# Optimization experiments

Hardware: AMD Instinct MI355X
Metric: run time of the kernel (lower is better)

Reference implementation:

```python
import jax, jax.numpy as jnp
import numpy as np

FILTER_LENGTHS = (2, 4)  # from module: self.filter_length = [2, 4]


def _get_conv(signal, b, h, l, d_k, conv, w):
    # signal: [b, h*d_k, l] (raw reshape of [b,h,l,d_k], matching torch .reshape)
    f = max(FILTER_LENGTHS)
    pad = f // 2
    padded = jnp.pad(signal, ((0, 0), (0, 0), (pad, pad)))  # [b, d, l+f]
    # unfold(-1, f, 1)[:, :, :l, :] -> sliding windows, keep first l
    idx = jnp.arange(l)[:, None] + jnp.arange(f)[None, :]  # [l, f]
    seq = padded[:, :, idx]  # [b, d, l, f]
    # dynamic filter-length selection: w_f = filter_lengths * w, pick argmax
    f_s = jnp.asarray(FILTER_LENGTHS, dtype=signal.dtype)
    ind = jnp.argmax(f_s * w)
    chosen_len = jnp.asarray(FILTER_LENGTHS)[ind]
    mask = (jnp.arange(f) < chosen_len).astype(signal.dtype)  # [f]
    seq = seq * mask  # broadcast over [b, d, l, f]
    # depthwise-ish conv via einsum, then raw reshape (b, l, h*d_k) -> (b, h, l, d_k)
    out = jnp.einsum('bdlf,dof->blo', seq, conv)
    return out.reshape(b, h, l, d_k)


def reference(Q, K, V, attn_mask, conv_q, conv_k, w):
    b, h, l, d_k = Q.shape
    Qc = _get_conv(Q.reshape(b, h * d_k, l), b, h, l, d_k, conv_q, w) + Q
    Kc = _get_conv(K.reshape(b, h * d_k, l), b, h, l, d_k, conv_k, w) + K
    scores = jnp.einsum('bhqd,bhkd->bhqk', Qc, Kc) / np.sqrt(d_k).astype(Q.dtype)
    attn = jax.nn.softmax(scores, axis=-1)
    context = jnp.einsum('bhqk,bhkd->bhqd', attn, V)
    return context, attn


def setup_inputs() -> dict:
    key = jax.random.key(0)
    ks = jax.random.split(key, 6)
    b, h, l, d_k = 4, 8, 2048, 64
    d = h * d_k
    f = max(FILTER_LENGTHS)
    return {
        'Q': jax.random.normal(ks[0], (b, h, l, d_k), dtype=jnp.float32),
        'K': jax.random.normal(ks[1], (b, h, l, d_k), dtype=jnp.float32),
        'V': jax.random.normal(ks[2], (b, h, l, d_k), dtype=jnp.float32),
        'attn_mask': jnp.zeros((b, 1, l, l), dtype=bool),  # unused by forward
        'conv_q': jax.random.normal(ks[3], (d, d, f), dtype=jnp.float32),
        'conv_k': jax.random.normal(ks[4], (d, d, f), dtype=jnp.float32),
        'w': jax.random.normal(ks[5], (2,), dtype=jnp.float32),
    }
```

## Files before the change

### kernel.cpp

```cpp
#include <hip/hip_runtime.h>

typedef _Float16 f16;
typedef _Float16 f16x8 __attribute__((ext_vector_type(8)));
typedef float f32x16 __attribute__((ext_vector_type(16)));

#define MFMA32(A, B, C) __builtin_amdgcn_mfma_f32_32x32x16_f16(A, B, C, 0, 0, 0)

constexpr int Bb = 4, Hh = 8, Ll = 2048, Dk = 64, Dm = 512, BH = 32;
constexpr int LP = 2052;

constexpr size_t NW  = (size_t)512 * 2048;
constexpr size_t NST = (size_t)Bb * LP * 512;
constexpr size_t NFF = (size_t)BH * 64 * 4 * 64 * 8;
constexpr size_t NVF = (size_t)BH * 2 * 128 * 64 * 8;

constexpr size_t OFF_W  = 256;
constexpr size_t OFF_ST = OFF_W + 4 * NW * sizeof(f16);
constexpr size_t OFF_FF = OFF_ST + 4 * NST * sizeof(f16);
constexpr size_t OFF_VF = OFF_FF + 4 * NFF * sizeof(f16);

#define QSCALE 0.1803368801111204f

__device__ __forceinline__ void gload_lds16(const void* g, void* l) {
    __builtin_amdgcn_global_load_lds((const __attribute__((address_space(1))) unsigned int*)g,
                                     (__attribute__((address_space(3))) unsigned int*)l, 16, 0, 0);
}

__global__ void kprep_w(const float* __restrict__ convq, const float* __restrict__ convk,
                        const float* __restrict__ w, int* __restrict__ flag,
                        f16* __restrict__ wqh, f16* __restrict__ wql,
                        f16* __restrict__ wkh, f16* __restrict__ wkl) {
    const int len = (4.f * w[1] > 2.f * w[0]) ? 4 : 2;
    if (blockIdx.x == 0 && blockIdx.y == 0 && threadIdx.x == 0) *flag = len;
    int tid = blockIdx.x * 256 + threadIdx.x;
    int o = tid >> 9, c = tid & 511;
    const float* conv = blockIdx.y ? convk : convq;
    f16* dh = blockIdx.y ? wkh : wqh;
    f16* dl = blockIdx.y ? wkl : wql;
    const float4 v = *(const float4*)(conv + ((size_t)c * 512 + o) * 4);
    float vv[4] = {v.x, v.y, v.z, v.w};
#pragma unroll
    for (int f = 0; f < 4; ++f) {
        float x = (f < len) ? vv[f] : 0.f;
        f16 hi = (f16)x;
        f16 lo = (f16)(x - (float)hi);
        size_t idx = (size_t)o * 2048 + (f << 9) + c;
        dh[idx] = hi; dl[idx] = lo;
    }
}

__global__ void kprep_s(const float* __restrict__ Q, const float* __restrict__ K,
                        f16* __restrict__ stqh, f16* __restrict__ stql,
                        f16* __restrict__ stkh, f16* __restrict__ stkl) {
    __shared__ float tile[64][65];
    int z = blockIdx.z;
    int tensor = z >> 2, b = z & 3;
    const float* src = (tensor ? K : Q) + (size_t)b * Dm * Ll;
    f16* dh = (tensor ? stkh : stqh) + (size_t)b * LP * Dm;
    f16* dl = (tensor ? stkl : stql) + (size_t)b * LP * Dm;
    int j0 = blockIdx.x * 64, c0 = blockIdx.y * 64;
    int tl = threadIdx.x & 63, tg = threadIdx.x >> 6;
#pragma unroll
    for (int r = 0; r < 16; ++r) {
        int cl = (r << 2) + tg;
        int tabs = j0 + tl - 2;
        float v = (tabs >= 0 && tabs < Ll) ? src[(size_t)(c0 + cl) * Ll + tabs] : 0.f;
        tile[cl][tl] = v;
    }
    __syncthreads();
#pragma unroll
    for (int r = 0; r < 16; ++r) {
        int jl = (r << 2) + tg;
        int j = j0 + jl;
        if (j < LP) {
            float v = tile[tl][jl];
            f16 hi = (f16)v;
            f16 lo = (f16)(v - (float)hi);
            dh[(size_t)j * Dm + c0 + tl] = hi;
            dl[(size_t)j * Dm + c0 + tl] = lo;
        }
    }
}

__global__ void kprep_v(const float* __restrict__ V, f16* __restrict__ vf) {
    int bh = blockIdx.y, l0 = blockIdx.x * 128;
    int tid = threadIdx.x;
    const float* src = V + (size_t)bh * Ll * Dk;
#pragma unroll
    for (int s = 0; s < 4; ++s) {
        int g = s * 4 + (tid >> 6);
        int lane = tid & 63;
        int l16s = g >> 1, db = g & 1;
        int khalf = lane >> 5, lane31 = lane & 31;
        int d = db * 32 + lane31;
        f16x8 out;
#pragma unroll
        for (int j = 0; j < 8; ++j) {
            int l = l0 + l16s * 16 + khalf * 8 + j;
            out[j] = (f16)src[(size_t)l * Dk + d];
        }
        size_t idx = ((((size_t)bh * 2 + db) * 128 + (l0 >> 4) + l16s) * 64 + lane) * 8;
        *(f16x8*)(vf + idx) = out;
    }
}

__global__ __launch_bounds__(256, 2) void kconv(
    const float* __restrict__ Q, const float* __restrict__ K, const int* __restrict__ flag,
    const f16* __restrict__ stqh, const f16* __restrict__ stql,
    const f16* __restrict__ stkh, const f16* __restrict__ stkl,
    const f16* __restrict__ wqh, const f16* __restrict__ wql,
    const f16* __restrict__ wkh, const f16* __restrict__ wkl,
    f16* __restrict__ ffhq, f16* __restrict__ fflq,
    f16* __restrict__ ffhk, f16* __restrict__ fflk) {
    __shared__ f16 At[128 * 64], Bt[128 * 64];
    int id = blockIdx.x;
    int oTile = id & 3, tensor = (id >> 2) & 1;
    int tt = (id >> 3) & 15, b = (id >> 7) & 3;
    int tid = threadIdx.x;
    int wave = tid >> 6, lane = tid & 63;
    int wm = wave >> 1, wn = wave & 1;
    int lane31 = lane & 31, khalf = lane >> 5;
    int t0 = tt * 128, o0 = oTile * 128;
    const f16* sh = (tensor ? stkh : stqh) + (size_t)b * LP * Dm;
    const f16* sl = (tensor ? stkl : stql) + (size_t)b * LP * Dm;
    const f16* wh = tensor ? wkh : wqh;
    const f16* wl = tensor ? wkl : wql;
    const float* src = (tensor ? K : Q) + (size_t)b * Hh * Ll * Dk;
    f16* dh = (tensor ? ffhk : ffhq);
    f16* dl = (tensor ? fflk : fflq);
    const float scale = tensor ? 1.f : QSCALE;
    const int klen = (*flag) << 9;
    const int iters = (3 * klen) >> 6;

    f32x16 acc[2][2];
#pragma unroll
    for (int i = 0; i < 2; ++i)
#pragma unroll
        for (int j = 0; j < 2; ++j)
#pragma unroll
            for (int r = 0; r < 16; ++r) acc[i][j][r] = 0.f;

    for (int it = 0; it < iters; ++it) {
        int kp = it << 6;
        int p = (kp >= 2 * klen) ? 2 : (kp >= klen ? 1 : 0);
        int k0 = kp - p * klen;
        int f = k0 >> 9, c0 = k0 & 511;
        const f16* srcA = (p == 2) ? sl : sh;
        const f16* srcB = (p == 1) ? wl : wh;
        __syncthreads();
#pragma unroll
        for (int c = 0; c < 4; ++c) {
            int s = c * 256 + tid;
            int row = s >> 3;
            int gk = ((s & 7) ^ (row & 7)) * 8;
            gload_lds16(srcA + (size_t)(t0 + f + row) * 512 + c0 + gk, &At[s * 8]);
            gload_lds16(srcB + (size_t)(o0 + row) * 2048 + k0 + gk, &Bt[s * 8]);
        }
        __syncthreads();
#pragma unroll
        for (int kk = 0; kk < 4; ++kk) {
            int cc = (kk << 1) + khalf;
            f16x8 av[2], bv[2];
#pragma unroll
            for (int i = 0; i < 2; ++i) {
                int row = wm * 64 + i * 32 + lane31;
                av[i] = *(const f16x8*)&At[(row * 8 + (cc ^ (row & 7))) * 8];
            }
#pragma unroll
            for (int j = 0; j < 2; ++j) {
                int row = wn * 64 + j * 32 + lane31;
                bv[j] = *(const f16x8*)&Bt[(row * 8 + (cc ^ (row & 7))) * 8];
            }
#pragma unroll
            for (int i = 0; i < 2; ++i)
#pragma unroll
                for (int j = 0; j < 2; ++j)
                    acc[i][j] = MFMA32(av[i], bv[j], acc[i][j]);
        }
    }
#pragma unroll
    for (int i = 0; i < 2; ++i)
#pragma unroll
        for (int j = 0; j < 2; ++j)
#pragma unroll
            for (int r = 0; r < 16; ++r) {
                int trow = t0 + wm * 64 + i * 32 + (r & 3) + ((r >> 2) << 3) + (khalf << 2);
                int ocol = o0 + wn * 64 + j * 32 + lane31;
                int h = trow >> 8;
                int l = ((trow & 255) << 3) + (ocol >> 6);
                int d = ocol & 63;
                float v2 = (acc[i][j][r] + src[((size_t)h * Ll + l) * Dk + d]) * scale;
                f16 hi = (f16)v2;
                f16 lo = (f16)(v2 - (float)hi);
                size_t idx = ((((size_t)(b * 8 + h) * 64 + (l >> 5)) * 4 + (d >> 4)) * 64
                              + ((d >> 3) & 1) * 32 + (l & 31)) * 8 + (d & 7);
                dh[idx] = hi; dl[idx] = lo;
            }
}

__global__ __launch_bounds__(256, 4) void kattn(
    const f16* __restrict__ qfh, const f16* __restrict__ qfl,
    const f16* __restrict__ kfh, const f16* __restrict__ kfl,
    const f16* __restrict__ vf,
    float* __restrict__ ctx_out, float* __restrict__ attn_out) {
    __shared__ __align__(16) char smem[16384];
    float (*combuf)[32][64] = (float (*)[32][64])smem;
    f16 (*ptile)[32][40] = (f16 (*)[32][40])smem;
    int id = blockIdx.x;
    int bh = (id & 7) * 4 + (id >> 8);
    int qt = (id >> 3) & 31;
    int wave = threadIdx.x >> 6, lane = threadIdx.x & 63;
    int qg = wave >> 1, kg = wave & 1;
    int lane31 = lane & 31, khalf = lane >> 5;
    int q0 = qt * 64 + qg * 32;

    f16x8 a_h[4], a_l[4];
    {
        size_t qb = ((size_t)bh * 64 + qt * 2 + qg) * 4;
#pragma unroll
        for (int ks = 0; ks < 4; ++ks) {
            a_h[ks] = *(const f16x8*)(qfh + ((qb + ks) * 64 + lane) * 8);
            a_l[ks] = *(const f16x8*)(qfl + ((qb + ks) * 64 + lane) * 8);
        }
    }
    const f16* kbh = kfh + (size_t)bh * 131072;
    const f16* kbl = kfl + (size_t)bh * 131072;
    const int ch0 = kg * 32, ch1 = ch0 + 32;

    float m[16], s[16];
#pragma unroll
    for (int r = 0; r < 16; ++r) { m[r] = -3.0e38f; s[r] = 0.f; }

#pragma unroll 2
    for (int ch = ch0; ch < ch1; ++ch) {
        f32x16 acc;
#pragma unroll
        for (int r = 0; r < 16; ++r) acc[r] = 0.f;
        size_t kb = (size_t)ch * 2048 + lane * 8;
#pragma unroll
        for (int ks = 0; ks < 4; ++ks) {
            f16x8 kh8 = *(const f16x8*)(kbh + kb + ks * 512);
            f16x8 kl8 = *(const f16x8*)(kbl + kb + ks * 512);
            acc = MFMA32(a_h[ks], kh8, acc);
            acc = MFMA32(a_h[ks], kl8, acc);
            acc = MFMA32(a_l[ks], kh8, acc);
        }
#pragma unroll
        for (int r = 0; r < 16; ++r) {
            float v = acc[r];
            float d = v - m[r];
            float e = exp2f(-fabsf(d));
            bool gt = d > 0.f;
            s[r] = gt ? __fmaf_rn(s[r], e, 1.f) : (s[r] + e);
            m[r] = gt ? v : m[r];
        }
    }
#pragma unroll
    for (int r = 0; r < 16; ++r) {
        float mm = m[r], ss = s[r];
#pragma unroll
        for (int off = 1; off < 32; off <<= 1) {
            float mo = __shfl_xor(mm, off, 64);
            float so = __shfl_xor(ss, off, 64);
            float mn = fmaxf(mm, mo);
            ss = ss * exp2f(mm - mn) + so * exp2f(mo - mn);
            mm = mn;
        }
        m[r] = mm; s[r] = ss;
    }
    if (kg == 1) {
#pragma unroll
        for (int r = 0; r < 16; ++r) {
            combuf[qg][r][lane] = m[r];
            combuf[qg][16 + r][lane] = s[r];
        }
    }
    __syncthreads();
    if (kg == 0) {
#pragma unroll
        for (int r = 0; r < 16; ++r) {
            float m1 = combuf[qg][r][lane];
            float s1 = combuf[qg][16 + r][lane];
            float mn = fmaxf(m[r], m1);
            float ss = s[r] * exp2f(m[r] - mn) + s1 * exp2f(m1 - mn);
            m[r] = mn; s[r] = 1.f / ss;
            combuf[qg][r][lane] = mn;
            combuf[qg][16 + r][lane] = s[r];
        }
    }
    __syncthreads();
    if (kg == 1) {
#pragma unroll
        for (int r = 0; r < 16; ++r) {
            m[r] = combuf[qg][r][lane];
            s[r] = combuf[qg][16 + r][lane];
        }
    }
    __syncthreads();

    f32x16 ctx[2];
#pragma unroll
    for (int n = 0; n < 2; ++n)
#pragma unroll
        for (int r = 0; r < 16; ++r) ctx[n][r] = 0.f;

    const size_t base_q = ((size_t)bh * Ll + q0) * Ll + lane31;

    for (int ch = ch0; ch < ch1; ++ch) {
        f32x16 acc;
#pragma unroll
        for (int r = 0; r < 16; ++r) acc[r] = 0.f;
        size_t kb = (size_t)ch * 2048 + lane * 8;
#pragma unroll
        for (int ks = 0; ks < 4; ++ks) {
            f16x8 kh8 = *(const f16x8*)(kbh + kb + ks * 512);
            f16x8 kl8 = *(const f16x8*)(kbl + kb + ks * 512);
            acc = MFMA32(a_h[ks], kh8, acc);
            acc = MFMA32(a_h[ks], kl8, acc);
            acc = MFMA32(a_l[ks], kh8, acc);
        }
#pragma unroll
        for (int r = 0; r < 16; ++r) {
            float p = exp2f(acc[r] - m[r]) * s[r];
            int row = (r & 3) + ((r >> 2) << 3) + (khalf << 2);
            attn_out[base_q + (size_t)row * Ll + ch * 32] = p;
            ptile[wave][row][lane31] = (f16)p;
        }
        __asm__ volatile("s_waitcnt lgkmcnt(0)" ::: "memory");
#pragma unroll
        for (int ks2 = 0; ks2 < 2; ++ks2) {
            f16x8 pa = *(const f16x8*)&ptile[wave][lane31][ks2 * 16 + khalf * 8];
#pragma unroll
            for (int n = 0; n < 2; ++n) {
                size_t off = ((((size_t)bh * 2 + n) * 128 + ch * 2 + ks2) * 64 + lane) * 8;
                f16x8 vb = *(const f16x8*)(vf + off);
                ctx[n] = MFMA32(pa, vb, ctx[n]);
            }
        }
    }
    __syncthreads();
    if (kg == 1) {
#pragma unroll
        for (int n = 0; n < 2; ++n)
#pragma unroll
            for (int r = 0; r < 16; ++r) combuf[qg][n * 16 + r][lane] = ctx[n][r];
    }
    __syncthreads();
    if (kg == 0) {
#pragma unroll
        for (int n = 0; n < 2; ++n)
#pragma unroll
            for (int r = 0; r < 16; ++r) {
                float v = ctx[n][r] + combuf[qg][n * 16 + r][lane];
                int row = (r & 3) + ((r >> 2) << 3) + (khalf << 2);
                ctx_out[((size_t)bh * Ll + q0 + row) * Dk + n * 32 + lane31] = v;
            }
    }
}

extern "C" void kernel_launch(void* const* d_in, const int* in_sizes, int n_in,
                              void* d_out, int out_size, void* d_ws, size_t ws_size,
                              hipStream_t stream) {
    const float* Q = (const float*)d_in[0];
    const float* K = (const float*)d_in[1];
    const float* V = (const float*)d_in[2];
    const float* convq = (const float*)d_in[4];
    const float* convk = (const float*)d_in[5];
    const float* w = (const float*)d_in[6];

    char* ws = (char*)d_ws;
    int* flag = (int*)ws;
    f16* wqh = (f16*)(ws + OFF_W);
    f16* wql = wqh + NW;
    f16* wkh = wql + NW;
    f16* wkl = wkh + NW;
    f16* stqh = (f16*)(ws + OFF_ST);
    f16* stql = stqh + NST;
    f16* stkh = stql + NST;
    f16* stkl = stkh + NST;
    f16* ffhq = (f16*)(ws + OFF_FF);
    f16* fflq = ffhq + NFF;
    f16* ffhk = fflq + NFF;
    f16* fflk = ffhk + NFF;
    f16* vf = (f16*)(ws + OFF_VF);

    float* ctx_out = (float*)d_out;
    float* attn_out = ctx_out + (size_t)BH * Ll * Dk;

    kprep_w<<<dim3(1024, 2), 256, 0, stream>>>(convq, convk, w, flag, wqh, wql, wkh, wkl);
    kprep_s<<<dim3(33, 8, 8), 256, 0, stream>>>(Q, K, stqh, stql, stkh, stkl);
    kprep_v<<<dim3(16, 32), 256, 0, stream>>>(V, vf);
    kconv<<<dim3(512), 256, 0, stream>>>(Q, K, flag, stqh, stql, stkh, stkl,
                                         wqh, wql, wkh, wkl, ffhq, fflq, ffhk, fflk);
    kattn<<<dim3(1024), 256, 0, stream>>>(ffhq, fflq, ffhk, fflk, vf, ctx_out, attn_out);
}
```

Baseline: 1.081 ms.

## Merge prep kernels, double-buffer conv GEMM, pair chunks and vectorize attn stores

Merges the three preprocessing kernels into one launch that dispatches on block index. The conv GEMM gets double-buffered LDS with the next stage's loads issued before compute, and its block-to-tile mapping is remapped. The attention kernel now processes two 32-key chunks per iteration with a combined online-softmax update. Probabilities are staged in an fp32 LDS tile so the attn output is written with float4 row-contiguous stores instead of scattered scalar stores. The occupancy hint drops from 4 to 3 blocks per CU, and the larger LDS use may reduce occupancy.

```diff
diff --git a/kernel.cpp b/kernel.cpp
--- a/kernel.cpp
+++ b/kernel.cpp
@@ -26,81 +26,88 @@
                                      (__attribute__((address_space(3))) unsigned int*)l, 16, 0, 0);
 }
 
-__global__ void kprep_w(const float* __restrict__ convq, const float* __restrict__ convk,
-                        const float* __restrict__ w, int* __restrict__ flag,
-                        f16* __restrict__ wqh, f16* __restrict__ wql,
-                        f16* __restrict__ wkh, f16* __restrict__ wkl) {
-    const int len = (4.f * w[1] > 2.f * w[0]) ? 4 : 2;
-    if (blockIdx.x == 0 && blockIdx.y == 0 && threadIdx.x == 0) *flag = len;
-    int tid = blockIdx.x * 256 + threadIdx.x;
-    int o = tid >> 9, c = tid & 511;
-    const float* conv = blockIdx.y ? convk : convq;
-    f16* dh = blockIdx.y ? wkh : wqh;
-    f16* dl = blockIdx.y ? wkl : wql;
-    const float4 v = *(const float4*)(conv + ((size_t)c * 512 + o) * 4);
-    float vv[4] = {v.x, v.y, v.z, v.w};
-#pragma unroll
-    for (int f = 0; f < 4; ++f) {
-        float x = (f < len) ? vv[f] : 0.f;
-        f16 hi = (f16)x;
-        f16 lo = (f16)(x - (float)hi);
-        size_t idx = (size_t)o * 2048 + (f << 9) + c;
-        dh[idx] = hi; dl[idx] = lo;
-    }
-}
-
-__global__ void kprep_s(const float* __restrict__ Q, const float* __restrict__ K,
-                        f16* __restrict__ stqh, f16* __restrict__ stql,
-                        f16* __restrict__ stkh, f16* __restrict__ stkl) {
+__global__ void kprep(const float* __restrict__ Q, const float* __restrict__ K,
+                      const float* __restrict__ V,
+                      const float* __restrict__ convq, const float* __restrict__ convk,
+                      const float* __restrict__ w, int* __restrict__ flag,
+                      f16* __restrict__ wqh, f16* __restrict__ wql,
+                      f16* __restrict__ wkh, f16* __restrict__ wkl,
+                      f16* __restrict__ stqh, f16* __restrict__ stql,
+                      f16* __restrict__ stkh, f16* __restrict__ stkl,
+                      f16* __restrict__ vf) {
     __shared__ float tile[64][65];
-    int z = blockIdx.z;
-    int tensor = z >> 2, b = z & 3;
-    const float* src = (tensor ? K : Q) + (size_t)b * Dm * Ll;
-    f16* dh = (tensor ? stkh : stqh) + (size_t)b * LP * Dm;
-    f16* dl = (tensor ? stkl : stql) + (size_t)b * LP * Dm;
-    int j0 = blockIdx.x * 64, c0 = blockIdx.y * 64;
-    int tl = threadIdx.x & 63, tg = threadIdx.x >> 6;
-#pragma unroll
-    for (int r = 0; r < 16; ++r) {
-        int cl = (r << 2) + tg;
-        int tabs = j0 + tl - 2;
-        float v = (tabs >= 0 && tabs < Ll) ? src[(size_t)(c0 + cl) * Ll + tabs] : 0.f;
-        tile[cl][tl] = v;
-    }
-    __syncthreads();
-#pragma unroll
-    for (int r = 0; r < 16; ++r) {
-        int jl = (r << 2) + tg;
-        int j = j0 + jl;
-        if (j < LP) {
-            float v = tile[tl][jl];
-            f16 hi = (f16)v;
-            f16 lo = (f16)(v - (float)hi);
-            dh[(size_t)j * Dm + c0 + tl] = hi;
-            dl[(size_t)j * Dm + c0 + tl] = lo;
-        }
-    }
-}
-
-__global__ void kprep_v(const float* __restrict__ V, f16* __restrict__ vf) {
-    int bh = blockIdx.y, l0 = blockIdx.x * 128;
-    int tid = threadIdx.x;
-    const float* src = V + (size_t)bh * Ll * Dk;
-#pragma unroll
-    for (int s = 0; s < 4; ++s) {
-        int g = s * 4 + (tid >> 6);
-        int lane = tid & 63;
-        int l16s = g >> 1, db = g & 1;
-        int khalf = lane >> 5, lane31 = lane & 31;
-        int d = db * 32 + lane31;
-        f16x8 out;
-#pragma unroll
-        for (int j = 0; j < 8; ++j) {
-            int l = l0 + l16s * 16 + khalf * 8 + j;
-            out[j] = (f16)src[(size_t)l * Dk + d];
-        }
-        size_t idx = ((((size_t)bh * 2 + db) * 128 + (l0 >> 4) + l16s) * 64 + lane) * 8;
-        *(f16x8*)(vf + idx) = out;
+    int id = blockIdx.x;
+    if (id < 2048) {
+        const int len = (4.f * w[1] > 2.f * w[0]) ? 4 : 2;
+        if (id == 0 && threadIdx.x == 0) *flag = len;
+        int part = id >> 10;
+        int tid = (id & 1023) * 256 + threadIdx.x;
+        int o = tid >> 9, c = tid & 511;
+        const float* conv = part ? convk : convq;
+        f16* dh = part ? wkh : wqh;
+        f16* dl = part ? wkl : wql;
+        const float4 v = *(const float4*)(conv + ((size_t)c * 512 + o) * 4);
+        float vv[4] = {v.x, v.y, v.z, v.w};
+#pragma unroll
+        for (int f = 0; f < 4; ++f) {
+            float x = (f < len) ? vv[f] : 0.f;
+            f16 hi = (f16)x;
+            f16 lo = (f16)(x - (float)hi);
+            size_t idx = (size_t)o * 2048 + (f << 9) + c;
+            dh[idx] = hi; dl[idx] = lo;
+        }
+    } else if (id < 4160) {
+        int sid = id - 2048;
+        int jb = sid % 33;
+        int rest = sid / 33;
+        int cb = rest & 7, z = rest >> 3;
+        int tensor = z >> 2, b = z & 3;
+        const float* src = (tensor ? K : Q) + (size_t)b * Dm * Ll;
+        f16* dh = (tensor ? stkh : stqh) + (size_t)b * LP * Dm;
+        f16* dl = (tensor ? stkl : stql) + (size_t)b * LP * Dm;
+        int j0 = jb * 64, c0 = cb * 64;
+        int tl = threadIdx.x & 63, tg = threadIdx.x >> 6;
+#pragma unroll
+        for (int r = 0; r < 16; ++r) {
+            int cl = (r << 2) + tg;
+            int tabs = j0 + tl - 2;
+            float v = (tabs >= 0 && tabs < Ll) ? src[(size_t)(c0 + cl) * Ll + tabs] : 0.f;
+            tile[cl][tl] = v;
+        }
+        __syncthreads();
+#pragma unroll
+        for (int r = 0; r < 16; ++r) {
+            int jl = (r << 2) + tg;
+            int j = j0 + jl;
+            if (j < LP) {
+                float v = tile[tl][jl];
+                f16 hi = (f16)v;
+                f16 lo = (f16)(v - (float)hi);
+                dh[(size_t)j * Dm + c0 + tl] = hi;
+                dl[(size_t)j * Dm + c0 + tl] = lo;
+            }
+        }
+    } else {
+        int vid = id - 4160;
+        int bh = vid >> 4, l0 = (vid & 15) * 128;
+        int tid = threadIdx.x;
+        const float* src = V + (size_t)bh * Ll * Dk;
+#pragma unroll
+        for (int s = 0; s < 4; ++s) {
+            int g = s * 4 + (tid >> 6);
+            int lane = tid & 63;
+            int l16s = g >> 1, db = g & 1;
+            int khalf = lane >> 5, lane31 = lane & 31;
+            int d = db * 32 + lane31;
+            f16x8 out;
+#pragma unroll
+            for (int j = 0; j < 8; ++j) {
+                int l = l0 + l16s * 16 + khalf * 8 + j;
+                out[j] = (f16)src[(size_t)l * Dk + d];
+            }
+            size_t idx = ((((size_t)bh * 2 + db) * 128 + (l0 >> 4) + l16s) * 64 + lane) * 8;
+            *(f16x8*)(vf + idx) = out;
+        }
     }
 }
 
@@ -112,10 +119,11 @@
     const f16* __restrict__ wkh, const f16* __restrict__ wkl,
     f16* __restrict__ ffhq, f16* __restrict__ fflq,
     f16* __restrict__ ffhk, f16* __restrict__ fflk) {
-    __shared__ f16 At[128 * 64], Bt[128 * 64];
+    __shared__ f16 At[2][128 * 64], Bt[2][128 * 64];
     int id = blockIdx.x;
-    int oTile = id & 3, tensor = (id >> 2) & 1;
-    int tt = (id >> 3) & 15, b = (id >> 7) & 3;
+    int oTile = (id >> 3) & 3;
+    int gg = (id >> 5) * 8 + (id & 7);
+    int tt = gg & 15, b = (gg >> 4) & 3, tensor = gg >> 6;
     int tid = threadIdx.x;
     int wave = tid >> 6, lane = tid & 63;
     int wm = wave >> 1, wn = wave & 1;
@@ -140,23 +148,27 @@
 #pragma unroll
             for (int r = 0; r < 16; ++r) acc[i][j][r] = 0.f;
 
-    for (int it = 0; it < iters; ++it) {
+    auto stage = [&](int it, int buf) {
         int kp = it << 6;
         int p = (kp >= 2 * klen) ? 2 : (kp >= klen ? 1 : 0);
         int k0 = kp - p * klen;
         int f = k0 >> 9, c0 = k0 & 511;
-        const f16* srcA = (p == 2) ? sl : sh;
-        const f16* srcB = (p == 1) ? wl : wh;
+        const f16* sA = (p == 2) ? sl : sh;
+        const f16* sB = (p == 1) ? wl : wh;
+#pragma unroll
+        for (int c = 0; c < 4; ++c) {
+            int sIdx = c * 256 + tid;
+            int row = sIdx >> 3;
+            int gk = ((sIdx & 7) ^ (row & 7)) * 8;
+            gload_lds16(sA + (size_t)(t0 + f + row) * 512 + c0 + gk, &At[buf][sIdx * 8]);
+            gload_lds16(sB + (size_t)(o0 + row) * 2048 + k0 + gk, &Bt[buf][sIdx * 8]);
+        }
+    };
+    stage(0, 0);
+    for (int it = 0; it < iters; ++it) {
+        int cur = it & 1;
         __syncthreads();
-#pragma unroll
-        for (int c = 0; c < 4; ++c) {
-            int s = c * 256 + tid;
-            int row = s >> 3;
-            int gk = ((s & 7) ^ (row & 7)) * 8;
-            gload_lds16(srcA + (size_t)(t0 + f + row) * 512 + c0 + gk, &At[s * 8]);
-            gload_lds16(srcB + (size_t)(o0 + row) * 2048 + k0 + gk, &Bt[s * 8]);
-        }
-        __syncthreads();
+        if (it + 1 < iters) stage(it + 1, cur ^ 1);
 #pragma unroll
         for (int kk = 0; kk < 4; ++kk) {
             int cc = (kk << 1) + khalf;
@@ -164,12 +176,12 @@
 #pragma unroll
             for (int i = 0; i < 2; ++i) {
                 int row = wm * 64 + i * 32 + lane31;
-                av[i] = *(const f16x8*)&At[(row * 8 + (cc ^ (row & 7))) * 8];
+                av[i] = *(const f16x8*)&At[cur][(row * 8 + (cc ^ (row & 7))) * 8];
             }
 #pragma unroll
             for (int j = 0; j < 2; ++j) {
                 int row = wn * 64 + j * 32 + lane31;
-                bv[j] = *(const f16x8*)&Bt[(row * 8 + (cc ^ (row & 7))) * 8];
+                bv[j] = *(const f16x8*)&Bt[cur][(row * 8 + (cc ^ (row & 7))) * 8];
             }
 #pragma unroll
             for (int i = 0; i < 2; ++i)
@@ -198,14 +210,13 @@
             }
 }
 
-__global__ __launch_bounds__(256, 4) void kattn(
+__global__ __launch_bounds__(256, 3) void kattn(
     const f16* __restrict__ qfh, const f16* __restrict__ qfl,
     const f16* __restrict__ kfh, const f16* __restrict__ kfl,
     const f16* __restrict__ vf,
     float* __restrict__ ctx_out, float* __restrict__ attn_out) {
-    __shared__ __align__(16) char smem[16384];
+    __shared__ __align__(16) float smem[4][32][66];
     float (*combuf)[32][64] = (float (*)[32][64])smem;
-    f16 (*ptile)[32][40] = (f16 (*)[32][40])smem;
     int id = blockIdx.x;
     int bh = (id & 7) * 4 + (id >> 8);
     int qt = (id >> 3) & 31;
@@ -225,34 +236,33 @@
     }
     const f16* kbh = kfh + (size_t)bh * 131072;
     const f16* kbl = kfl + (size_t)bh * 131072;
-    const int ch0 = kg * 32, ch1 = ch0 + 32;
 
     float m[16], s[16];
 #pragma unroll
     for (int r = 0; r < 16; ++r) { m[r] = -3.0e38f; s[r] = 0.f; }
 
-#pragma unroll 2
-    for (int ch = ch0; ch < ch1; ++ch) {
-        f32x16 acc;
-#pragma unroll
-        for (int r = 0; r < 16; ++r) acc[r] = 0.f;
+    for (int pr = 0; pr < 16; ++pr) {
+        int ch = kg * 32 + pr * 2;
+        f32x16 accA, accB;
+#pragma unroll
+        for (int r = 0; r < 16; ++r) { accA[r] = 0.f; accB[r] = 0.f; }
         size_t kb = (size_t)ch * 2048 + lane * 8;
 #pragma unroll
         for (int ks = 0; ks < 4; ++ks) {
-            f16x8 kh8 = *(const f16x8*)(kbh + kb + ks * 512);
-            f16x8 kl8 = *(const f16x8*)(kbl + kb + ks * 512);
-            acc = MFMA32(a_h[ks], kh8, acc);
-            acc = MFMA32(a_h[ks], kl8, acc);
-            acc = MFMA32(a_l[ks], kh8, acc);
-        }
-#pragma unroll
-        for (int r = 0; r < 16; ++r) {
-            float v = acc[r];
-            float d = v - m[r];
-            float e = exp2f(-fabsf(d));
-            bool gt = d > 0.f;
-            s[r] = gt ? __fmaf_rn(s[r], e, 1.f) : (s[r] + e);
-            m[r] = gt ? v : m[r];
+            f16x8 khA = *(const f16x8*)(kbh + kb + ks * 512);
+            f16x8 klA = *(const f16x8*)(kbl + kb + ks * 512);
+            f16x8 khB = *(const f16x8*)(kbh + kb + 2048 + ks * 512);
+            f16x8 klB = *(const f16x8*)(kbl + kb + 2048 + ks * 512);
+            accA = MFMA32(a_h[ks], khA, accA);  accB = MFMA32(a_h[ks], khB, accB);
+            accA = MFMA32(a_h[ks], klA, accA);  accB = MFMA32(a_h[ks], klB, accB);
+            accA = MFMA32(a_l[ks], khA, accA);  accB = MFMA32(a_l[ks], khB, accB);
+        }
+#pragma unroll
+        for (int r = 0; r < 16; ++r) {
+            float va = accA[r], vb = accB[r];
+            float mx = fmaxf(fmaxf(va, vb), m[r]);
+            s[r] = __fmaf_rn(s[r], exp2f(m[r] - mx), exp2f(va - mx) + exp2f(vb - mx));
+            m[r] = mx;
         }
     }
 #pragma unroll
@@ -304,35 +314,50 @@
 #pragma unroll
         for (int r = 0; r < 16; ++r) ctx[n][r] = 0.f;
 
-    const size_t base_q = ((size_t)bh * Ll + q0) * Ll + lane31;
-
-    for (int ch = ch0; ch < ch1; ++ch) {
-        f32x16 acc;
-#pragma unroll
-        for (int r = 0; r < 16; ++r) acc[r] = 0.f;
+    float* pt = &smem[wave][0][0];
+    float* arow = attn_out + ((size_t)(bh * Ll + q0 + lane31)) * Ll + kg * 1024 + khalf * 8;
+
+    for (int pr = 0; pr < 16; ++pr) {
+        int ch = kg * 32 + pr * 2;
+        f32x16 accA, accB;
+#pragma unroll
+        for (int r = 0; r < 16; ++r) { accA[r] = 0.f; accB[r] = 0.f; }
         size_t kb = (size_t)ch * 2048 + lane * 8;
 #pragma unroll
         for (int ks = 0; ks < 4; ++ks) {
-            f16x8 kh8 = *(const f16x8*)(kbh + kb + ks * 512);
-            f16x8 kl8 = *(const f16x8*)(kbl + kb + ks * 512);
-            acc = MFMA32(a_h[ks], kh8, acc);
-            acc = MFMA32(a_h[ks], kl8, acc);
-            acc = MFMA32(a_l[ks], kh8, acc);
-        }
-#pragma unroll
-        for (int r = 0; r < 16; ++r) {
-            float p = exp2f(acc[r] - m[r]) * s[r];
+            f16x8 khA = *(const f16x8*)(kbh + kb + ks * 512);
+            f16x8 klA = *(const f16x8*)(kbl + kb + ks * 512);
+            f16x8 khB = *(const f16x8*)(kbh + kb + 2048 + ks * 512);
+            f16x8 klB = *(const f16x8*)(kbl + kb + 2048 + ks * 512);
+            accA = MFMA32(a_h[ks], khA, accA);  accB = MFMA32(a_h[ks], khB, accB);
+            accA = MFMA32(a_h[ks], klA, accA);  accB = MFMA32(a_h[ks], klB, accB);
+            accA = MFMA32(a_l[ks], khA, accA);  accB = MFMA32(a_l[ks], khB, accB);
+        }
+#pragma unroll
+        for (int r = 0; r < 16; ++r) {
             int row = (r & 3) + ((r >> 2) << 3) + (khalf << 2);
-            attn_out[base_q + (size_t)row * Ll + ch * 32] = p;
-            ptile[wave][row][lane31] = (f16)p;
+            float p0 = exp2f(accA[r] - m[r]) * s[r];
+            float p1 = exp2f(accB[r] - m[r]) * s[r];
+            pt[row * 66 + lane31] = p0;
+            pt[row * 66 + 34 + lane31] = p1;
         }
         __asm__ volatile("s_waitcnt lgkmcnt(0)" ::: "memory");
 #pragma unroll
-        for (int ks2 = 0; ks2 < 2; ++ks2) {
-            f16x8 pa = *(const f16x8*)&ptile[wave][lane31][ks2 * 16 + khalf * 8];
+        for (int ks2 = 0; ks2 < 4; ++ks2) {
+            int k0 = ks2 * 16 + khalf * 8;
+            int c0 = k0 + ((k0 >> 5) << 1);
+            const float2* rp = (const float2*)(pt + lane31 * 66 + c0);
+            float2 w0 = rp[0], w1 = rp[1], w2 = rp[2], w3 = rp[3];
+            float4 s0 = {w0.x, w0.y, w1.x, w1.y};
+            float4 s1 = {w2.x, w2.y, w3.x, w3.y};
+            *(float4*)(arow + pr * 64 + ks2 * 16) = s0;
+            *(float4*)(arow + pr * 64 + ks2 * 16 + 4) = s1;
+            f16x8 pa = {(f16)w0.x, (f16)w0.y, (f16)w1.x, (f16)w1.y,
+                        (f16)w2.x, (f16)w2.y, (f16)w3.x, (f16)w3.y};
+            int l16 = kg * 64 + pr * 4 + ks2;
 #pragma unroll
             for (int n = 0; n < 2; ++n) {
-                size_t off = ((((size_t)bh * 2 + n) * 128 + ch * 2 + ks2) * 64 + lane) * 8;
+                size_t off = (((size_t)bh * 2 + n) * 128 + l16) * 512 + lane * 8;
                 f16x8 vb = *(const f16x8*)(vf + off);
                 ctx[n] = MFMA32(pa, vb, ctx[n]);
             }
@@ -387,9 +412,9 @@
     float* ctx_out = (float*)d_out;
     float* attn_out = ctx_out + (size_t)BH * Ll * Dk;
 
-    kprep_w<<<dim3(1024, 2), 256, 0, stream>>>(convq, convk, w, flag, wqh, wql, wkh, wkl);
-    kprep_s<<<dim3(33, 8, 8), 256, 0, stream>>>(Q, K, stqh, stql, stkh, stkl);
-    kprep_v<<<dim3(16, 32), 256, 0, stream>>>(V, vf);
+    kprep<<<dim3(4672), 256, 0, stream>>>(Q, K, V, convq, convk, w, flag,
+                                          wqh, wql, wkh, wkl,
+                                          stqh, stql, stkh, stkl, vf);
     kconv<<<dim3(512), 256, 0, stream>>>(Q, K, flag, stqh, stql, stkh, stkl,
                                          wqh, wql, wkh, wkl, ffhq, fflq, ffhk, fflk);
     kattn<<<dim3(1024), 256, 0, stream>>>(ffhq, fflq, ffhk, fflk, vf, ctx_out, attn_out);
```

New measurement: 1.161 ms. +7.4%, slower.
